# Optimization experiments

Measured on AMD Instinct MI355X. Metric: run time of the kernel, lower is better.

## Reference

```python
import jax, jax.numpy as jnp
import numpy as np

DT = 0.0166667
BATCH, NJ, NM = 16384, 64, 8


def setup_inputs() -> dict:
    key = jax.random.key(0)
    ks = jax.random.split(key, 10)
    SS = jax.random.normal(ks[0], (BATCH, NJ, 2), jnp.float32) * 0.1
    Alphas = jax.random.uniform(ks[1], (BATCH, NJ, NM), dtype=jnp.float32)
    # Positive, physically plausible muscle params (stiffness, rest length, moment arm)
    K0s = jax.random.uniform(ks[2], (NJ, NM), dtype=jnp.float32) * 2.0 + 1.0
    K1s = jax.random.uniform(ks[3], (NJ, NM), dtype=jnp.float32) * 2.0 + 0.5
    L0s = jax.random.uniform(ks[4], (NJ, NM), dtype=jnp.float32) * 0.10 + 0.05
    L1s = jax.random.uniform(ks[5], (NJ, NM), dtype=jnp.float32) * 0.10 + 0.05
    Ms = jax.random.uniform(ks[6], (NJ, NM), dtype=jnp.float32) * 0.04 + 0.01
    I = jax.random.uniform(ks[7], (NJ,), dtype=jnp.float32) * 0.5 + 0.5
    Bj = jax.random.uniform(ks[8], (NJ,), dtype=jnp.float32) * 0.5 + 0.1
    Kj = jax.random.uniform(ks[9], (NJ,), dtype=jnp.float32) * 2.0 + 0.5
    return {"SS": SS, "Alphas": Alphas, "K0s": K0s, "K1s": K1s, "L0s": L0s,
            "L1s": L1s, "Ms": Ms, "I": I, "Bj": Bj, "Kj": Kj}


def _forward(SS, Alphas, K0s, K1s, L0s, L1s, Ms, I, Bj, Kj):
    b, j = SS.shape[0], SS.shape[1]
    Alphas = jnp.clip(Alphas, 0.0, 1.0)                              # [b,j,m]
    muscle_SS = SS[:, :, :, None] * Ms[None, :, None, :]             # [b,j,2,m]
    # Effective joint stiffness
    Kact = (K0s + K1s * Alphas) * (Ms * Ms)                          # [b,j,m]
    Ksum = Kact.sum(-1)                                              # [b,j]
    A10 = -(Ksum + Kj) / I
    Dmp = 2.0 * jnp.sqrt(Ksum * I)                                   # critical damping term
    A11 = -(Dmp + Bj) / I
    zeros = jnp.zeros((b, j), jnp.float32)
    ones = jnp.ones((b, j), jnp.float32)
    Amat = jnp.stack([jnp.stack([zeros, ones], -1),
                      jnp.stack([A10, A11], -1)], -2)                # [b,j,2,2]
    # Muscle force -> joint torque input matrix
    B_F = (K0s + K1s * Alphas) * (L0s + L1s * Alphas - jnp.abs(muscle_SS[:, :, 0, :])) \
          + K1s * L1s * Alphas * Alphas                              # [b,j,m]
    B10 = (B_F * Ms / I[None, :, None]).sum(-1)                      # [b,j]
    B11 = ones / I
    Bmat = jnp.stack([jnp.stack([zeros, zeros], -1),
                      jnp.stack([B10, B11], -1)], -2)                # [b,j,2,2]
    # Augmented 6x6 system for exact ZOH/linear-interp integration
    Z22 = jnp.zeros((b, j, 2, 2), jnp.float32)
    I2 = jnp.broadcast_to(jnp.eye(2, dtype=jnp.float32), (b, j, 2, 2))
    M = jnp.concatenate([
        jnp.concatenate([Amat * DT, Bmat * DT, Z22], -1),
        jnp.concatenate([Z22, Z22, I2], -1),
        jnp.zeros((b, j, 2, 6), jnp.float32),
    ], -2)                                                           # [b,j,6,6]
    expM = jax.vmap(jax.scipy.linalg.expm)(M.reshape(-1, 6, 6)).reshape(b, j, 6, 6)
    Ad = expM[:, :, :2, :2]
    Bd1 = expM[:, :, :2, 4:6]
    Bd0 = expM[:, :, :2, 2:4] - Bd1
    U0 = jnp.zeros((b, j, 2), jnp.float32).at[:, :, 0].set(1.0)      # U1 == U0 in source
    SSout = (jnp.einsum('bjik,bjk->bji', Ad, SS)
             + jnp.einsum('bjik,bjk->bji', Bd0, U0)
             + jnp.einsum('bjik,bjk->bji', Bd1, U0))                 # [b,j,2]
    return SSout


def reference(SS, Alphas, K0s, K1s, L0s, L1s, Ms, I, Bj, Kj):
    SSout = _forward(SS, Alphas, K0s, K1s, L0s, L1s, Ms, I, Bj, Kj)
    return SSout[:, :, 0], SSout
```

## Files before the change

### kernel.cpp

```cpp
#include <hip/hip_runtime.h>


constexpr int BATCH = 16384;
constexpr int NJ = 64;
constexpr int NM = 8;

__global__ __launch_bounds__(256) void bilinear_joints_kernel(
    const float* __restrict__ SS,
    const float* __restrict__ Alphas,
    const float* __restrict__ K0s,
    const float* __restrict__ K1s,
    const float* __restrict__ L0s,
    const float* __restrict__ L1s,
    const float* __restrict__ Ms,
    const float* __restrict__ Iarr,
    const float* __restrict__ Bjarr,
    const float* __restrict__ Kjarr,
    float* __restrict__ out0,
    float* __restrict__ out1)
{
    const float dt = 0.0166667f;
    const int idx = blockIdx.x * blockDim.x + threadIdx.x;
    if (idx >= BATCH * NJ) return;
    const int j = idx & (NJ - 1);

    const float2 ss  = *reinterpret_cast<const float2*>(SS + 2 * idx);
    const float4 a0v = *reinterpret_cast<const float4*>(Alphas + 8 * idx);
    const float4 a1v = *reinterpret_cast<const float4*>(Alphas + 8 * idx + 4);
    const float4 K0a = *reinterpret_cast<const float4*>(K0s + 8 * j);
    const float4 K0b = *reinterpret_cast<const float4*>(K0s + 8 * j + 4);
    const float4 K1a = *reinterpret_cast<const float4*>(K1s + 8 * j);
    const float4 K1b = *reinterpret_cast<const float4*>(K1s + 8 * j + 4);
    const float4 L0a = *reinterpret_cast<const float4*>(L0s + 8 * j);
    const float4 L0b = *reinterpret_cast<const float4*>(L0s + 8 * j + 4);
    const float4 L1a = *reinterpret_cast<const float4*>(L1s + 8 * j);
    const float4 L1b = *reinterpret_cast<const float4*>(L1s + 8 * j + 4);
    const float4 Msa = *reinterpret_cast<const float4*>(Ms + 8 * j);
    const float4 Msb = *reinterpret_cast<const float4*>(Ms + 8 * j + 4);

    const float Iv   = Iarr[j];
    const float Bjv  = Bjarr[j];
    const float Kjv  = Kjarr[j];
    const float invI = 1.0f / Iv;

    const float al[NM] = {a0v.x, a0v.y, a0v.z, a0v.w, a1v.x, a1v.y, a1v.z, a1v.w};
    const float k0[NM] = {K0a.x, K0a.y, K0a.z, K0a.w, K0b.x, K0b.y, K0b.z, K0b.w};
    const float k1[NM] = {K1a.x, K1a.y, K1a.z, K1a.w, K1b.x, K1b.y, K1b.z, K1b.w};
    const float l0[NM] = {L0a.x, L0a.y, L0a.z, L0a.w, L0b.x, L0b.y, L0b.z, L0b.w};
    const float l1[NM] = {L1a.x, L1a.y, L1a.z, L1a.w, L1b.x, L1b.y, L1b.z, L1b.w};
    const float ms[NM] = {Msa.x, Msa.y, Msa.z, Msa.w, Msb.x, Msb.y, Msb.z, Msb.w};

    const float absSS0 = fabsf(ss.x);

    float ksum = 0.0f, bacc = 0.0f;
#pragma unroll
    for (int m = 0; m < NM; ++m) {
        const float a  = fminf(fmaxf(al[m], 0.0f), 1.0f);
        const float kk = fmaf(k1[m], a, k0[m]);
        const float mv = ms[m];
        ksum = fmaf(kk * mv, mv, ksum);
        const float lt = fmaf(l1[m], a, l0[m]) - absSS0 * mv;
        const float bf = fmaf(kk, lt, k1[m] * l1[m] * a * a);
        bacc = fmaf(bf, mv, bacc);
    }

    const float B10 = bacc * invI;
    const float A10 = -(ksum + Kjv) * invI;
    const float Dmp = 2.0f * sqrtf(ksum * Iv);
    const float A11 = -(Dmp + Bjv) * invI;

    const float t = A11 * dt;
    const float s = 0.5f * t;
    const float d = -A10 * dt * dt;
    const float Delta = s * s - d;
    const float es = __expf(s);

    float alphaE, betaE, alphaP, betaP;
    if (Delta < 0.0f) {
        const float r  = sqrtf(-Delta);
        float si, co;
        __sincosf(r, &si, &co);
        const float sinc = (r > 1e-6f) ? si / r : 1.0f;
        betaE  = es * sinc;
        alphaE = es * co - betaE * s;
        const float invd = 1.0f / d;
        betaP = (s * es * sinc - es * co + 1.0f) * invd;
        const float ref1 = (s * (es * co - 1.0f) + r * r * es * sinc) * invd;
        alphaP = ref1 - betaP * s;
    } else {
        const float r  = sqrtf(Delta);
        const float er = __expf(r);
        const float ier = 1.0f / er;
        const float ch = 0.5f * (er + ier);
        const float sh = 0.5f * (er - ier);
        const float sinch = (r > 1e-6f) ? sh / r : 1.0f;
        betaE  = es * sinch;
        alphaE = es * ch - betaE * s;
        const float lam1 = s + r, lam2 = s - r;
        const float f1 = (fabsf(lam1) > 1e-6f) ? expm1f(lam1) / lam1 : 1.0f + 0.5f * lam1;
        const float f2 = (fabsf(lam2) > 1e-6f) ? expm1f(lam2) / lam2 : 1.0f + 0.5f * lam2;
        if (r > 1e-5f) {
            betaP = (f1 - f2) * (0.5f / r);
        } else {
            const float s2 = s * s;
            betaP = (s2 > 1e-12f) ? (es * (s - 1.0f) + 1.0f) / s2 : 0.5f;
        }
        alphaP = 0.5f * (f1 + f2) - betaP * s;
    }

    const float Ad00 = alphaE;
    const float Ad01 = betaE * dt;
    const float Ad10 = betaE * A10 * dt;
    const float Ad11 = alphaE + betaE * A11 * dt;

    const float c1 = B10 * dt;
    const float w0 = betaP * dt * c1;
    const float w1 = (alphaP + betaP * A11 * dt) * c1;

    const float o0 = fmaf(Ad00, ss.x, fmaf(Ad01, ss.y, w0));
    const float o1 = fmaf(Ad10, ss.x, fmaf(Ad11, ss.y, w1));

    out0[idx] = o0;
    float2 o; o.x = o0; o.y = o1;
    *reinterpret_cast<float2*>(out1 + 2 * idx) = o;
}

extern "C" void kernel_launch(void* const* d_in, const int* in_sizes, int n_in,
                              void* d_out, int out_size, void* d_ws, size_t ws_size,
                              hipStream_t stream) {
    const float* SS     = (const float*)d_in[0];
    const float* Alphas = (const float*)d_in[1];
    const float* K0s    = (const float*)d_in[2];
    const float* K1s    = (const float*)d_in[3];
    const float* L0s    = (const float*)d_in[4];
    const float* L1s    = (const float*)d_in[5];
    const float* Msp    = (const float*)d_in[6];
    const float* Iarr   = (const float*)d_in[7];
    const float* Bjarr  = (const float*)d_in[8];
    const float* Kjarr  = (const float*)d_in[9];

    float* out0 = (float*)d_out;
    float* out1 = out0 + BATCH * NJ;

    const int total = BATCH * NJ;
    const int block = 256;
    const int grid = (total + block - 1) / block;

    bilinear_joints_kernel<<<grid, block, 0, stream>>>(
        SS, Alphas, K0s, K1s, L0s, L1s, Msp, Iarr, Bjarr, Kjarr, out0, out1);
}
```

Measured before the change: 98.73 us.

## Precompute per-joint muscle coefficients in shared memory and simplify exponential math

Each block's first 64 threads precompute per-joint polynomial coefficients (expanded stiffness and force terms in alpha) plus scaled constants into shared memory. The per-element loop then drops to a few FMAs per muscle instead of recomputing products of K0/K1/L0/L1/Ms. Divisions become hardware reciprocal approximations and expm1f is replaced with exp products reused from already computed exponentials. This adds a __syncthreads and per-block setup work, and the approximate reciprocal plus the expm1 replacement with a raised threshold may reduce accuracy.

```diff
diff --git a/kernel.cpp b/kernel.cpp
--- a/kernel.cpp
+++ b/kernel.cpp
@@ -4,6 +4,9 @@
 constexpr int BATCH = 16384;
 constexpr int NJ = 64;
 constexpr int NM = 8;
+constexpr float DT = 0.0166667f;
+
+__device__ __forceinline__ float rcpf(float x) { return __builtin_amdgcn_rcpf(x); }
 
 __global__ __launch_bounds__(256) void bilinear_joints_kernel(
     const float* __restrict__ SS,
@@ -19,103 +22,141 @@
     float* __restrict__ out0,
     float* __restrict__ out1)
 {
-    const float dt = 0.0166667f;
-    const int idx = blockIdx.x * blockDim.x + threadIdx.x;
+    __shared__ float sj[NJ][36];
+
+    const int tid = threadIdx.x;
+
+    if (tid < NJ) {
+        const int j = tid;
+        const float4 K0a = *reinterpret_cast<const float4*>(K0s + 8 * j);
+        const float4 K0b = *reinterpret_cast<const float4*>(K0s + 8 * j + 4);
+        const float4 K1a = *reinterpret_cast<const float4*>(K1s + 8 * j);
+        const float4 K1b = *reinterpret_cast<const float4*>(K1s + 8 * j + 4);
+        const float4 L0a = *reinterpret_cast<const float4*>(L0s + 8 * j);
+        const float4 L0b = *reinterpret_cast<const float4*>(L0s + 8 * j + 4);
+        const float4 L1a = *reinterpret_cast<const float4*>(L1s + 8 * j);
+        const float4 L1b = *reinterpret_cast<const float4*>(L1s + 8 * j + 4);
+        const float4 Msa = *reinterpret_cast<const float4*>(Ms + 8 * j);
+        const float4 Msb = *reinterpret_cast<const float4*>(Ms + 8 * j + 4);
+
+        const float k0[NM] = {K0a.x, K0a.y, K0a.z, K0a.w, K0b.x, K0b.y, K0b.z, K0b.w};
+        const float k1[NM] = {K1a.x, K1a.y, K1a.z, K1a.w, K1b.x, K1b.y, K1b.z, K1b.w};
+        const float l0[NM] = {L0a.x, L0a.y, L0a.z, L0a.w, L0b.x, L0b.y, L0b.z, L0b.w};
+        const float l1[NM] = {L1a.x, L1a.y, L1a.z, L1a.w, L1b.x, L1b.y, L1b.z, L1b.w};
+        const float ms[NM] = {Msa.x, Msa.y, Msa.z, Msa.w, Msb.x, Msb.y, Msb.z, Msb.w};
+
+        float C0 = 0.0f, D0 = 0.0f;
+#pragma unroll
+        for (int m = 0; m < NM; ++m) {
+            const float mv  = ms[m];
+            const float ms2 = mv * mv;
+            sj[j][m]      = k1[m] * ms2;
+            sj[j][8 + m]  = mv * fmaf(k0[m], l1[m], k1[m] * l0[m]);
+            sj[j][16 + m] = 2.0f * mv * k1[m] * l1[m];
+            C0 = fmaf(k0[m], ms2, C0);
+            D0 = fmaf(mv * k0[m], l0[m], D0);
+        }
+        const float Iv   = Iarr[j];
+        const float Bjv  = Bjarr[j];
+        const float Kjv  = Kjarr[j];
+        const float invI = rcpf(Iv);
+        const float ddk  = invI * DT * DT;
+        const float sc   = -0.5f * invI * DT;
+        sj[j][24] = C0;
+        sj[j][25] = D0;
+        sj[j][26] = ddk;
+        sj[j][27] = Kjv * ddk;
+        sj[j][28] = sc;
+        sj[j][29] = Bjv * sc;
+        sj[j][30] = Iv;
+        sj[j][31] = invI * DT;
+    }
+    __syncthreads();
+
+    const int idx = blockIdx.x * blockDim.x + tid;
     if (idx >= BATCH * NJ) return;
-    const int j = idx & (NJ - 1);
+    const int j = tid & (NJ - 1);
 
     const float2 ss  = *reinterpret_cast<const float2*>(SS + 2 * idx);
     const float4 a0v = *reinterpret_cast<const float4*>(Alphas + 8 * idx);
     const float4 a1v = *reinterpret_cast<const float4*>(Alphas + 8 * idx + 4);
-    const float4 K0a = *reinterpret_cast<const float4*>(K0s + 8 * j);
-    const float4 K0b = *reinterpret_cast<const float4*>(K0s + 8 * j + 4);
-    const float4 K1a = *reinterpret_cast<const float4*>(K1s + 8 * j);
-    const float4 K1b = *reinterpret_cast<const float4*>(K1s + 8 * j + 4);
-    const float4 L0a = *reinterpret_cast<const float4*>(L0s + 8 * j);
-    const float4 L0b = *reinterpret_cast<const float4*>(L0s + 8 * j + 4);
-    const float4 L1a = *reinterpret_cast<const float4*>(L1s + 8 * j);
-    const float4 L1b = *reinterpret_cast<const float4*>(L1s + 8 * j + 4);
-    const float4 Msa = *reinterpret_cast<const float4*>(Ms + 8 * j);
-    const float4 Msb = *reinterpret_cast<const float4*>(Ms + 8 * j + 4);
 
-    const float Iv   = Iarr[j];
-    const float Bjv  = Bjarr[j];
-    const float Kjv  = Kjarr[j];
-    const float invI = 1.0f / Iv;
+    const float4* p = reinterpret_cast<const float4*>(&sj[j][0]);
+    const float4 c1a = p[0], c1b = p[1];
+    const float4 d1a = p[2], d1b = p[3];
+    const float4 d2a = p[4], d2b = p[5];
+    const float4 s0  = p[6], s1  = p[7];
+    const float C0 = s0.x, D0 = s0.y, ddk = s0.z, dd0 = s0.w;
+    const float sc = s1.x, sb = s1.y, Iv = s1.z, bscale = s1.w;
 
     const float al[NM] = {a0v.x, a0v.y, a0v.z, a0v.w, a1v.x, a1v.y, a1v.z, a1v.w};
-    const float k0[NM] = {K0a.x, K0a.y, K0a.z, K0a.w, K0b.x, K0b.y, K0b.z, K0b.w};
-    const float k1[NM] = {K1a.x, K1a.y, K1a.z, K1a.w, K1b.x, K1b.y, K1b.z, K1b.w};
-    const float l0[NM] = {L0a.x, L0a.y, L0a.z, L0a.w, L0b.x, L0b.y, L0b.z, L0b.w};
-    const float l1[NM] = {L1a.x, L1a.y, L1a.z, L1a.w, L1b.x, L1b.y, L1b.z, L1b.w};
-    const float ms[NM] = {Msa.x, Msa.y, Msa.z, Msa.w, Msb.x, Msb.y, Msb.z, Msb.w};
+    const float c1[NM] = {c1a.x, c1a.y, c1a.z, c1a.w, c1b.x, c1b.y, c1b.z, c1b.w};
+    const float d1[NM] = {d1a.x, d1a.y, d1a.z, d1a.w, d1b.x, d1b.y, d1b.z, d1b.w};
+    const float d2[NM] = {d2a.x, d2a.y, d2a.z, d2a.w, d2b.x, d2b.y, d2b.z, d2b.w};
 
-    const float absSS0 = fabsf(ss.x);
-
-    float ksum = 0.0f, bacc = 0.0f;
+    float ks = 0.0f, bb = 0.0f;
 #pragma unroll
     for (int m = 0; m < NM; ++m) {
-        const float a  = fminf(fmaxf(al[m], 0.0f), 1.0f);
-        const float kk = fmaf(k1[m], a, k0[m]);
-        const float mv = ms[m];
-        ksum = fmaf(kk * mv, mv, ksum);
-        const float lt = fmaf(l1[m], a, l0[m]) - absSS0 * mv;
-        const float bf = fmaf(kk, lt, k1[m] * l1[m] * a * a);
-        bacc = fmaf(bf, mv, bacc);
+        const float a = fminf(fmaxf(al[m], 0.0f), 1.0f);
+        ks = fmaf(a, c1[m], ks);
+        bb = fmaf(a, fmaf(a, d2[m], d1[m]), bb);
     }
+    const float absSS0 = fabsf(ss.x);
+    const float Ksum = C0 + ks;
+    const float bacc = D0 + bb - absSS0 * Ksum;
 
-    const float B10 = bacc * invI;
-    const float A10 = -(ksum + Kjv) * invI;
-    const float Dmp = 2.0f * sqrtf(ksum * Iv);
-    const float A11 = -(Dmp + Bjv) * invI;
-
-    const float t = A11 * dt;
-    const float s = 0.5f * t;
-    const float d = -A10 * dt * dt;
-    const float Delta = s * s - d;
-    const float es = __expf(s);
+    const float d   = fmaf(Ksum, ddk, dd0);
+    const float Dmp = 2.0f * sqrtf(Ksum * Iv);
+    const float s   = fmaf(Dmp, sc, sb);
+    const float Delta = fmaf(s, s, -d);
+    const float es  = __expf(s);
 
     float alphaE, betaE, alphaP, betaP;
     if (Delta < 0.0f) {
-        const float r  = sqrtf(-Delta);
+        const float r = sqrtf(-Delta);
         float si, co;
         __sincosf(r, &si, &co);
-        const float sinc = (r > 1e-6f) ? si / r : 1.0f;
-        betaE  = es * sinc;
-        alphaE = es * co - betaE * s;
-        const float invd = 1.0f / d;
-        betaP = (s * es * sinc - es * co + 1.0f) * invd;
-        const float ref1 = (s * (es * co - 1.0f) + r * r * es * sinc) * invd;
+        const float esco = es * co;
+        const float essi = es * si;
+        const float sinc = (r > 1e-6f) ? essi * rcpf(r) : es;
+        betaE  = sinc;
+        alphaE = esco - sinc * s;
+        const float invd = rcpf(d);
+        betaP  = fmaf(s, sinc, 1.0f - esco) * invd;
+        const float ref1 = fmaf(s, esco - 1.0f, essi * r) * invd;
         alphaP = ref1 - betaP * s;
     } else {
-        const float r  = sqrtf(Delta);
-        const float er = __expf(r);
-        const float ier = 1.0f / er;
-        const float ch = 0.5f * (er + ier);
-        const float sh = 0.5f * (er - ier);
-        const float sinch = (r > 1e-6f) ? sh / r : 1.0f;
+        const float r   = sqrtf(Delta);
+        const float er  = __expf(r);
+        const float ier = rcpf(er);
+        const float ch  = 0.5f * (er + ier);
+        const float sh  = 0.5f * (er - ier);
+        const float sinch = (r > 1e-6f) ? sh * rcpf(r) : 1.0f;
         betaE  = es * sinch;
         alphaE = es * ch - betaE * s;
         const float lam1 = s + r, lam2 = s - r;
-        const float f1 = (fabsf(lam1) > 1e-6f) ? expm1f(lam1) / lam1 : 1.0f + 0.5f * lam1;
-        const float f2 = (fabsf(lam2) > 1e-6f) ? expm1f(lam2) / lam2 : 1.0f + 0.5f * lam2;
+        const float f1 = (fabsf(lam1) > 1e-4f) ? (es * er - 1.0f) * rcpf(lam1)
+                                               : fmaf(0.5f, lam1, 1.0f);
+        const float f2 = (fabsf(lam2) > 1e-4f) ? (es * ier - 1.0f) * rcpf(lam2)
+                                               : fmaf(0.5f, lam2, 1.0f);
         if (r > 1e-5f) {
-            betaP = (f1 - f2) * (0.5f / r);
+            betaP = (f1 - f2) * 0.5f * rcpf(r);
         } else {
             const float s2 = s * s;
-            betaP = (s2 > 1e-12f) ? (es * (s - 1.0f) + 1.0f) / s2 : 0.5f;
+            betaP = (s2 > 1e-12f) ? (fmaf(es, s - 1.0f, 1.0f)) * rcpf(s2) : 0.5f;
         }
         alphaP = 0.5f * (f1 + f2) - betaP * s;
     }
 
+    constexpr float INVDT = 1.0f / DT;
     const float Ad00 = alphaE;
-    const float Ad01 = betaE * dt;
-    const float Ad10 = betaE * A10 * dt;
-    const float Ad11 = alphaE + betaE * A11 * dt;
+    const float Ad01 = betaE * DT;
+    const float Ad10 = -betaE * d * INVDT;
+    const float Ad11 = fmaf(2.0f * betaE, s, alphaE);
 
-    const float c1 = B10 * dt;
-    const float w0 = betaP * dt * c1;
-    const float w1 = (alphaP + betaP * A11 * dt) * c1;
+    const float c1v = bacc * bscale;
+    const float w0  = betaP * DT * c1v;
+    const float w1  = fmaf(2.0f * betaP, s, alphaP) * c1v;
 
     const float o0 = fmaf(Ad00, ss.x, fmaf(Ad01, ss.y, w0));
     const float o1 = fmaf(Ad10, ss.x, fmaf(Ad11, ss.y, w1));
```

Result: no change. 99.65 us (+0.9%).
